# Performance work log

Hardware: AMD Instinct MI355X
Metric: run time of the kernel (lower is better)

## Reference

```python
import jax, jax.numpy as jnp
import numpy as np

NUM_CLASSES = 80
C_OUT = 81
SCORE_THR = 0.02
IOU_THR = 0.45
TOPK = 1000
IMG_MAX = 320.0
STRIDES = [16, 32, 64, 107, 160, 320]
MIN_SIZES = [48, 100, 150, 202, 253, 304]
MAX_SIZES = [100, 150, 202, 253, 304, 320]
FEAT = [20, 10, 5, 3, 2, 1]
MAX_RATIO = float(abs(np.log(0.016)))


def _base_anchors(level):
    base = float(MIN_SIZES[level])
    scales = np.array([1.0, np.sqrt(MAX_SIZES[level] / MIN_SIZES[level])])
    ratios = np.array([1.0, 0.5, 2.0, 1.0 / 3.0, 3.0])
    h_ratios = np.sqrt(ratios)
    w_ratios = 1.0 / h_ratios
    # scale_major=False: scales vary along rows
    ws = (base * scales[:, None] * w_ratios[None, :]).reshape(-1)
    hs = (base * scales[:, None] * h_ratios[None, :]).reshape(-1)
    c = STRIDES[level] / 2.0
    ba = np.stack([c - 0.5 * ws, c - 0.5 * hs, c + 0.5 * ws, c + 0.5 * hs], -1)
    return ba[[0, 5, 1, 2, 3, 4]]  # index_select reorder, 6 anchors/loc


def _priors(level):
    ba = _base_anchors(level)
    f, s = FEAT[level], STRIDES[level]
    sx = np.arange(f, dtype=np.float64) * s
    xx = np.tile(sx, f)
    yy = np.repeat(sx, f)
    shifts = np.stack([xx, yy, xx, yy], -1)  # [f*f,4]
    return (ba[None, :, :] + shifts[:, None, :]).reshape(-1, 4).astype(np.float32)


PRIORS = [jnp.asarray(_priors(i)) for i in range(6)]


def delta2bbox(priors, deltas):
    stds = jnp.array([0.1, 0.1, 0.2, 0.2], dtype=deltas.dtype)
    d = deltas * stds
    pxy = (priors[:, :2] + priors[:, 2:]) * 0.5
    pwh = priors[:, 2:] - priors[:, :2]
    dwh = jnp.clip(d[:, 2:], -MAX_RATIO, MAX_RATIO)
    gxy = pxy + pwh * d[:, :2]
    gwh = pwh * jnp.exp(dwh)
    boxes = jnp.concatenate([gxy - 0.5 * gwh, gxy + 0.5 * gwh], -1)
    return jnp.clip(boxes, 0.0, IMG_MAX)


def _nms_keep(boxes, valid, iou_thr):
    # greedy NMS over score-sorted boxes; returns bool keep mask
    K = boxes.shape[0]
    area = (boxes[:, 2] - boxes[:, 0]) * (boxes[:, 3] - boxes[:, 1])
    lt = jnp.maximum(boxes[:, None, :2], boxes[None, :, :2])
    rb = jnp.minimum(boxes[:, None, 2:], boxes[None, :, 2:])
    wh = jnp.clip(rb - lt, 0.0)
    inter = wh[..., 0] * wh[..., 1]
    iou = inter / (area[:, None] + area[None, :] - inter)
    ar = jnp.arange(K)

    def body(i, alive):
        sup = (iou[i] > iou_thr) & (ar > i) & alive[i]
        return alive & ~sup

    return jax.lax.fori_loop(0, K, body, valid)


def _single_image(cls_list, bb_list):
    boxes_l, scores_l, labels_l, valid_l = [], [], [], []
    for cls, bb, priors in zip(cls_list, bb_list, PRIORS):
        probs = jax.nn.softmax(cls.transpose(1, 2, 0).reshape(-1, C_OUT), axis=-1)[:, :NUM_CLASSES]
        flat = probs.reshape(-1)  # [N*80]
        k = min(TOPK, flat.shape[0])
        masked = jnp.where(flat > SCORE_THR, flat, -1.0)
        vals, idx = jax.lax.top_k(masked, k)
        valid = vals > SCORE_THR
        a_idx = idx // NUM_CLASSES
        lbl = idx % NUM_CLASSES
        deltas = bb.transpose(1, 2, 0).reshape(-1, 4)[a_idx]
        boxes = delta2bbox(priors[a_idx], deltas)
        boxes_l.append(boxes)
        scores_l.append(jnp.where(valid, vals, 0.0))
        labels_l.append(lbl)
        valid_l.append(valid)
    boxes = jnp.concatenate(boxes_l, 0)   # [K,4]
    scores = jnp.concatenate(scores_l, 0)
    labels = jnp.concatenate(labels_l, 0)
    valid = jnp.concatenate(valid_l, 0)

    # batched (class-aware) NMS via per-class coordinate offsets
    max_coord = boxes.max()
    offsets = labels.astype(boxes.dtype) * (max_coord + 1.0)
    boxes_nms = boxes + offsets[:, None]
    order = jnp.argsort(-jnp.where(valid, scores, -jnp.inf))
    boxes_s = boxes[order]
    scores_s = scores[order]
    labels_s = labels[order]
    valid_s = valid[order]
    keep = jax.lax.stop_gradient(
        _nms_keep(jax.lax.stop_gradient(boxes_nms[order]), valid_s, IOU_THR))
    dets = jnp.concatenate([boxes_s, scores_s[:, None]], -1) * keep[:, None].astype(boxes.dtype)
    return dets, labels_s, keep


def setup_inputs() -> dict:
    key = jax.random.key(0)
    ks = jax.random.split(key, 12)
    B = 4
    inp = {}
    for i, f in enumerate(FEAT):
        inp[f"cls{i}"] = jax.random.normal(ks[i], (B, 486, f, f), dtype=jnp.float32)
        inp[f"bb{i}"] = jax.random.normal(ks[6 + i], (B, 24, f, f), dtype=jnp.float32)
    return inp


def reference(cls0, cls1, cls2, cls3, cls4, cls5, bb0, bb1, bb2, bb3, bb4, bb5):
    def one(c0, c1, c2, c3, c4, c5, b0, b1, b2, b3, b4, b5):
        return _single_image([c0, c1, c2, c3, c4, c5], [b0, b1, b2, b3, b4, b5])
    dets, labels, keep = jax.vmap(one)(cls0, cls1, cls2, cls3, cls4, cls5,
                                       bb0, bb1, bb2, bb3, bb4, bb5)
    return dets, labels, keep
```

## Files before the change

kernel.cpp:

```cpp
#include <hip/hip_runtime.h>
#include <stdint.h>

#define NB 4
#define KTOT 5480
#define PER_IMG 258720
#define SCORE_THR 0.02f
#define IOU_THR 0.45f
#define REL_BASE 0x3CA3D70Bu
#define JCH 10
#define JSZ 548
#define ICH 11
#define NMSCAP 512

__constant__ int cFEAT[6]    = {20,10,5,3,2,1};
__constant__ int cSTRIDE[6]  = {16,32,64,107,160,320};
__constant__ int cMIN[6]     = {48,100,150,202,253,304};
__constant__ int cMAX[6]     = {100,150,202,253,304,320};
__constant__ int cNFLAT[6]   = {192000,48000,12000,4320,1920,480};
__constant__ int cFLATOFF[6] = {0,192000,240000,252000,256320,258240};
__constant__ int cKSEL[6]    = {1000,1000,1000,1000,1000,480};
__constant__ int cKOFF[6]    = {0,1000,2000,3000,4000,5000};
__constant__ double cRATIO[6] = {1.0,1.0,0.5,2.0,1.0/3.0,3.0};
__constant__ int eTLEV[14]   = {0,0,0,0,0,0,0,0,1,1,2,3,4,5};
__constant__ int eTCHK[14]   = {0,1,2,3,4,5,6,7,0,1,0,0,0,0};
__constant__ int eNCH[6]     = {8,2,1,1,1,1};

__device__ __forceinline__ unsigned long long mk_key(unsigned kb, int lev, unsigned idx) {
  return ((unsigned long long)kb << 21) |
         (unsigned long long)(0x1FFFFFu ^ (((unsigned)lev << 18) | idx));
}

__device__ __forceinline__ unsigned long long shfl64(unsigned long long x, int src) {
  int lo = __shfl((int)(unsigned)(x & 0xffffffffull), src);
  int hi = __shfl((int)(unsigned)(x >> 32), src);
  return ((unsigned long long)(unsigned)hi << 32) | (unsigned)lo;
}

__global__ __launch_bounds__(256) void k_softmax(
    const float* __restrict__ c0, const float* __restrict__ c1,
    const float* __restrict__ c2, const float* __restrict__ c3,
    const float* __restrict__ c4, const float* __restrict__ c5,
    float* __restrict__ scores, unsigned* __restrict__ ghist)
{
  int t = blockIdx.x;
  int b = t / 78, rem = t % 78;
  int lev, a, cb;
  if (rem < 42)      { lev = 0; a = rem / 7;        cb = (rem % 7) * 64; }
  else if (rem < 54) { lev = 1; a = (rem - 42) >> 1; cb = ((rem - 42) & 1) * 64; }
  else               { lev = 2 + (rem - 54) / 6; a = (rem - 54) % 6; cb = 0; }
  const float* cls = (lev==0)?c0:(lev==1)?c1:(lev==2)?c2:(lev==3)?c3:(lev==4)?c4:c5;
  int f = cFEAT[lev], ff = f * f;
  int ncell = ff - cb; if (ncell > 64) ncell = 64;

  __shared__ float tile[81 * 64];
  const float* base = cls + (size_t)(b * 486 + a * 81) * ff + cb;
  for (int t2 = threadIdx.x; t2 < 81 * 64; t2 += 256) {
    int c = t2 >> 6, cell = t2 & 63;
    if (cell < ncell)
      tile[(c << 6) | (cell ^ (c & 63))] = base[c * ff + cell];
  }
  __syncthreads();

  int lane = threadIdx.x & 63, w = threadIdx.x >> 6;
  unsigned* h = ghist + (size_t)(b * 6 + lev) * 8192;
  for (int cell = w; cell < ncell; cell += 4) {
    float v1 = tile[(lane << 6) | (cell ^ lane)];
    float v2 = (lane <= 16) ? tile[((lane + 64) << 6) | (cell ^ lane)]
                            : __uint_as_float(0xff800000u);
    float mx = fmaxf(v1, v2);
    #pragma unroll
    for (int m = 32; m; m >>= 1) mx = fmaxf(mx, __shfl_xor(mx, m));
    float e1 = expf(v1 - mx);
    float e2 = (lane <= 16) ? expf(v2 - mx) : 0.f;
    float sm = e1 + e2;
    #pragma unroll
    for (int m = 32; m; m >>= 1) sm += __shfl_xor(sm, m);
    int row = (cb + cell) * 6 + a;
    float* out = scores + (size_t)b * PER_IMG + cFLATOFF[lev] + row * 80;
    float p1 = e1 / sm;
    out[lane] = (p1 > SCORE_THR) ? p1 : -1.f;
    if (p1 > SCORE_THR)
      atomicAdd(&h[(__float_as_uint(p1) - REL_BASE) >> 13], 1u);
    if (lane < 16) {
      float p2 = e2 / sm;
      out[lane + 64] = (p2 > SCORE_THR) ? p2 : -1.f;
      if (p2 > SCORE_THR)
        atomicAdd(&h[(__float_as_uint(p2) - REL_BASE) >> 13], 1u);
    }
  }
}

__global__ __launch_bounds__(1024) void k_plan(
    const unsigned* __restrict__ ghist, unsigned* __restrict__ ctrl)
{
  int task = blockIdx.x;
  int lev = task % 6;
  int tid = threadIdx.x;
  if (lev == 5) { if (tid == 0) ctrl[task * 8] = 2u; return; }
  unsigned k = (unsigned)cKSEL[lev];
  const unsigned* h = ghist + (size_t)task * 8192;
  unsigned loc[8];
  unsigned ssum = 0;
  #pragma unroll
  for (int j = 0; j < 8; ++j) { loc[j] = h[tid * 8 + j]; ssum += loc[j]; }
  __shared__ unsigned sc[1024];
  sc[tid] = ssum;
  __syncthreads();
  for (int off = 1; off < 1024; off <<= 1) {
    unsigned cur = sc[tid];
    unsigned add = (tid + off < 1024) ? sc[tid + off] : 0u;
    __syncthreads();
    sc[tid] = cur + add;
    __syncthreads();
  }
  unsigned c = sc[0];
  if (c < k) { if (tid == 0) ctrl[task * 8] = 1u; return; }
  unsigned above = (tid == 1023) ? 0u : sc[tid + 1];
  unsigned run = above;
  #pragma unroll
  for (int j = 7; j >= 0; --j) {
    unsigned hj = loc[j];
    if (run < k && run + hj >= k) {
      ctrl[task * 8 + 0] = 0u;
      ctrl[task * 8 + 1] = (unsigned)(tid * 8 + j);
    }
    run += hj;
  }
}

__global__ __launch_bounds__(256) void k_emit2(
    const float* __restrict__ scores, unsigned* __restrict__ ctrl,
    unsigned long long* __restrict__ selkeys, unsigned long long* __restrict__ eqg)
{
  int b = blockIdx.x / 14, ent = blockIdx.x % 14;
  int lev = eTLEV[ent], chk = eTCHK[ent];
  int task = b * 6 + lev;
  int n = cNFLAT[lev];
  int tid = threadIdx.x;
  const float* s = scores + (size_t)b * PER_IMG + cFLATOFF[lev];
  unsigned long long* out = selkeys + (size_t)b * KTOT + cKOFF[lev];

  if (lev == 5) {
    for (int i = tid; i < n; i += 256) {
      float v = s[i];
      unsigned kb = (v > SCORE_THR) ? __float_as_uint(v) : 0u;
      out[i] = mk_key(kb, lev, (unsigned)i);
    }
    return;
  }

  __shared__ unsigned long long wbuf[1024];
  __shared__ unsigned long long ebuf[4096];
  __shared__ unsigned wcnt, ecnt, sbw, sbe;
  if (tid == 0) { wcnt = 0; ecnt = 0; }
  __syncthreads();

  unsigned mode = ctrl[task * 8];
  int csz = n / eNCH[lev];
  int start = chk * csz;
  const float4* s4 = (const float4*)(s + start);
  int n4 = csz >> 2;

  if (mode == 0u) {
    unsigned b1 = ctrl[task * 8 + 1];
    unsigned base_lo = REL_BASE + (b1 << 13);
    unsigned base_hi = base_lo + 8192u;
    #pragma unroll 4
    for (int i0 = tid; i0 < n4; i0 += 256) {
      float4 vv = s4[i0];
      #pragma unroll
      for (int e2 = 0; e2 < 4; ++e2) {
        float v = (e2==0)?vv.x:(e2==1)?vv.y:(e2==2)?vv.z:vv.w;
        if (v > SCORE_THR) {
          unsigned kb = __float_as_uint(v);
          unsigned idx = (unsigned)(start + i0 * 4 + e2);
          if (kb >= base_hi) {
            unsigned p = atomicAdd(&wcnt, 1u);
            if (p < 1024u) wbuf[p] = mk_key(kb, lev, idx);
          } else if (kb >= base_lo) {
            unsigned p = atomicAdd(&ecnt, 1u);
            if (p < 4096u) ebuf[p] = mk_key(kb, lev, idx);
          }
        }
      }
    }
  } else {
    #pragma unroll 4
    for (int i0 = tid; i0 < n4; i0 += 256) {
      float4 vv = s4[i0];
      #pragma unroll
      for (int e2 = 0; e2 < 4; ++e2) {
        float v = (e2==0)?vv.x:(e2==1)?vv.y:(e2==2)?vv.z:vv.w;
        if (v > SCORE_THR) {
          unsigned p = atomicAdd(&wcnt, 1u);
          if (p < 1024u) wbuf[p] = mk_key(__float_as_uint(v), lev,
                                          (unsigned)(start + i0 * 4 + e2));
        }
      }
    }
  }
  __syncthreads();
  if (tid == 0) {
    sbw = atomicAdd(&ctrl[task * 8 + 2], wcnt);
    sbe = atomicAdd(&ctrl[task * 8 + 3], ecnt);
  }
  __syncthreads();
  unsigned nw = (wcnt < 1024u) ? wcnt : 1024u;
  unsigned ne = (ecnt < 4096u) ? ecnt : 4096u;
  unsigned bw = sbw, be = sbe;
  for (unsigned t = tid; t < nw; t += 256) out[bw + t] = wbuf[t];
  for (unsigned t = tid; t < ne; t += 256) {
    unsigned g = be + t;
    if (g < 4096u) eqg[(size_t)task * 4096 + g] = ebuf[t];
  }
}

__global__ __launch_bounds__(1024) void k_finalize2(
    const float* __restrict__ scores, const unsigned* __restrict__ ctrl,
    unsigned long long* __restrict__ selkeys, const unsigned long long* __restrict__ eqg)
{
  int task = blockIdx.x;
  int b = task / 6, lev = task % 6;
  if (lev == 5) return;
  int tid = threadIdx.x;
  unsigned k = (unsigned)cKSEL[lev];
  int n = cNFLAT[lev];
  const float* s = scores + (size_t)b * PER_IMG + cFLATOFF[lev];
  unsigned long long* out = selkeys + (size_t)b * KTOT + cKOFF[lev];
  unsigned levtag = (unsigned)lev << 18;
  unsigned mode = ctrl[task * 8];

  __shared__ unsigned long long eqb[4096];
  __shared__ unsigned sc[1024];
  __shared__ unsigned sh_cnt, sh_eq, sh_byte, sh_r;

  if (mode == 0u) {
    unsigned cnt = ctrl[task * 8 + 2];
    unsigned e = ctrl[task * 8 + 3];
    unsigned need = k - cnt;
    if (e <= 4096u) {
      const unsigned long long* eq = eqg + (size_t)task * 4096;
      if (e == need) {
        for (unsigned t = tid; t < need; t += 1024) out[cnt + t] = eq[t];
        return;
      }
      unsigned P = 1; while (P < e) P <<= 1;
      for (unsigned t = tid; t < P; t += 1024) eqb[t] = (t < e) ? eq[t] : 0ull;
      __syncthreads();
      for (unsigned sz = 2; sz <= P; sz <<= 1)
        for (unsigned st = sz >> 1; st; st >>= 1) {
          for (unsigned w = tid; w < P / 2; w += 1024) {
            unsigned i = ((w & ~(st - 1)) << 1) | (w & (st - 1));
            unsigned l = i | st;
            bool up = ((i & sz) == 0);
            unsigned long long A = eqb[i], B = eqb[l];
            if ((A < B) == up) { eqb[i] = B; eqb[l] = A; }
          }
          __syncthreads();
        }
      for (unsigned t = tid; t < need; t += 1024) out[cnt + t] = eqb[t];
      return;
    }
  } else if (mode == 1u) {
    unsigned c = ctrl[task * 8 + 2];
    unsigned need = k - c;
    unsigned base = 0;
    for (int start = 0; start < n && base < need; start += 1024) {
      int i = start + tid;
      unsigned pred = (i < n && !(s[i] > SCORE_THR)) ? 1u : 0u;
      sc[tid] = pred;
      __syncthreads();
      for (int off = 1; off < 1024; off <<= 1) {
        unsigned add = (tid >= off) ? sc[tid - off] : 0u;
        unsigned v = sc[tid];
        __syncthreads();
        sc[tid] = v + add;
        __syncthreads();
      }
      unsigned incl = sc[tid];
      unsigned total = sc[1023];
      unsigned excl = incl - pred;
      if (pred && (base + excl) < need)
        out[c + base + excl] =
            (unsigned long long)(0x1FFFFFu ^ (levtag | (unsigned)i));
      __syncthreads();
      base += total;
    }
    return;
  }

  unsigned* hist = sc;
  unsigned* equ = (unsigned*)eqb;
  unsigned prefix = 0, r = k;
  for (int pass = 3; pass >= 0; --pass) {
    int shift = pass * 8;
    for (int i = tid; i < 256; i += 1024) hist[i] = 0;
    __syncthreads();
    for (int i = tid; i < n; i += 1024) {
      float v = s[i];
      unsigned kb = (v > SCORE_THR) ? __float_as_uint(v) : 0u;
      bool match = (pass == 3) || (((kb ^ prefix) >> (shift + 8)) == 0u);
      if (match) atomicAdd(&hist[(kb >> shift) & 255u], 1u);
    }
    __syncthreads();
    if (tid == 0) {
      unsigned cum = 0, byte = 0, rr = r;
      for (int bb = 255; bb >= 0; --bb) {
        unsigned hh = hist[bb];
        if (cum + hh >= r) { byte = (unsigned)bb; rr = r - cum; break; }
        cum += hh;
      }
      sh_byte = byte; sh_r = rr;
    }
    __syncthreads();
    prefix |= (sh_byte << shift);
    r = sh_r;
    __syncthreads();
  }
  unsigned Kstar = prefix;
  if (tid == 0) { sh_cnt = 0; sh_eq = 0; }
  __syncthreads();
  for (int i = tid; i < n; i += 1024) {
    float v = s[i];
    unsigned kb = (v > SCORE_THR) ? __float_as_uint(v) : 0u;
    if (kb > Kstar) {
      unsigned slot = atomicAdd(&sh_cnt, 1u);
      out[slot] = mk_key(kb, lev, (unsigned)i);
    } else if (kb == Kstar) {
      unsigned es = atomicAdd(&sh_eq, 1u);
      if (es < 4096u) equ[es] = (unsigned)i;
    }
  }
  __syncthreads();
  unsigned m = sh_cnt;
  unsigned e2 = (sh_eq < 4096u) ? sh_eq : 4096u;
  unsigned need2 = k - m;
  if (e2 > need2) {
    unsigned P = 1; while (P < e2) P <<= 1;
    for (unsigned t = tid; t < P; t += 1024) if (t >= e2) equ[t] = 0xFFFFFFFFu;
    __syncthreads();
    for (unsigned sz = 2; sz <= P; sz <<= 1)
      for (unsigned st = sz >> 1; st; st >>= 1) {
        for (unsigned w = tid; w < P / 2; w += 1024) {
          unsigned i = ((w & ~(st - 1)) << 1) | (w & (st - 1));
          unsigned l = i | st;
          bool up = ((i & sz) == 0);
          unsigned A = equ[i], B = equ[l];
          if ((A > B) == up) { equ[i] = B; equ[l] = A; }
        }
        __syncthreads();
      }
  }
  __syncthreads();
  for (unsigned t = tid; t < need2; t += 1024)
    out[m + t] = ((unsigned long long)Kstar << 21) |
                 (unsigned long long)(0x1FFFFFu ^ (levtag | equ[t]));
}

__global__ __launch_bounds__(512) void k_rank(
    const unsigned long long* __restrict__ selkeys, unsigned* __restrict__ rank_part)
{
  int blk = blockIdx.x;
  int jc = blk % JCH;
  int rest = blk / JCH;
  int ic = rest % ICH, b = rest / ICH;
  int tid = threadIdx.x;
  __shared__ __align__(16) unsigned long long sk[JSZ];
  const unsigned long long* keys = selkeys + (size_t)b * KTOT;
  for (int j = tid; j < JSZ; j += 512) sk[j] = keys[jc * JSZ + j];
  int i = ic * 512 + tid;
  unsigned long long mk = (i < KTOT) ? keys[i] : 0ull;
  __syncthreads();
  unsigned r = 0;
  const ulonglong2* sk2 = (const ulonglong2*)sk;
  #pragma unroll 8
  for (int j = 0; j < JSZ / 2; ++j) {
    ulonglong2 kk = sk2[j];
    r += (kk.x > mk) ? 1u : 0u;
    r += (kk.y > mk) ? 1u : 0u;
  }
  if (i < KTOT) rank_part[((size_t)jc * NB + b) * KTOT + i] = r;
}

__global__ __launch_bounds__(512) void k_decode(
    const unsigned long long* __restrict__ selkeys, const unsigned* __restrict__ rank_part,
    const float* __restrict__ g0, const float* __restrict__ g1,
    const float* __restrict__ g2, const float* __restrict__ g3,
    const float* __restrict__ g4, const float* __restrict__ g5,
    float* __restrict__ boxes, float* __restrict__ oscore,
    unsigned char* __restrict__ lab8, unsigned* __restrict__ obmax_u,
    float* __restrict__ outp)
{
  int b = blockIdx.x / ICH, ic = blockIdx.x % ICH;
  int tid = threadIdx.x;
  int i = ic * 512 + tid;
  __shared__ double ba[6][6][4];
  if (tid < 36) {
    int lev = tid / 6, a = tid % 6;
    double base = (double)cMIN[lev];
    double scl = (a == 1) ? sqrt((double)cMAX[lev] / (double)cMIN[lev]) : 1.0;
    double hr = sqrt(cRATIO[a]);
    double wr = 1.0 / hr;
    double wsz = base * scl * wr;
    double hsz = base * scl * hr;
    double cc = (double)cSTRIDE[lev] / 2.0;
    ba[lev][a][0] = cc - 0.5 * wsz;
    ba[lev][a][1] = cc - 0.5 * hsz;
    ba[lev][a][2] = cc + 0.5 * wsz;
    ba[lev][a][3] = cc + 0.5 * hsz;
  }
  __syncthreads();

  float lmax = 0.f;
  if (i < KTOT) {
    unsigned long long mk = selkeys[(size_t)b * KTOT + i];
    unsigned r = 0;
    #pragma unroll
    for (int jc = 0; jc < JCH; ++jc)
      r += rank_part[((size_t)jc * NB + b) * KTOT + i];
    unsigned tag = 0x1FFFFFu ^ (unsigned)(mk & 0x1FFFFFull);
    int lev = tag >> 18;
    int fi = tag & 0x3FFFF;
    unsigned vb2 = (unsigned)(mk >> 21);
    int valid = (vb2 != 0u);
    float score = valid ? __uint_as_float(vb2) : 0.f;
    int label = fi % 80;
    int arow = fi / 80;
    int a = arow % 6, cell = arow / 6;
    int f = cFEAT[lev], ff = f * f;
    int x = cell % f, y = cell / f;
    const float* gb = (lev==0)?g0:(lev==1)?g1:(lev==2)?g2:(lev==3)?g3:(lev==4)?g4:g5;
    const float* pb = gb + (size_t)(b * 24 + a * 4) * ff + y * f + x;
    float d0 = pb[0] * 0.1f, d1 = pb[ff] * 0.1f;
    float d2 = pb[2 * ff] * 0.2f, d3 = pb[3 * ff] * 0.2f;
    const float MR = (float)4.135166556742356;
    d2 = fminf(fmaxf(d2, -MR), MR);
    d3 = fminf(fmaxf(d3, -MR), MR);
    double shx = (double)(x * cSTRIDE[lev]);
    double shy = (double)(y * cSTRIDE[lev]);
    float p0 = (float)(ba[lev][a][0] + shx);
    float p1 = (float)(ba[lev][a][1] + shy);
    float p2 = (float)(ba[lev][a][2] + shx);
    float p3 = (float)(ba[lev][a][3] + shy);
    float pxc = (p0 + p2) * 0.5f, pyc = (p1 + p3) * 0.5f;
    float pw = p2 - p0, ph = p3 - p1;
    float gx = pxc + pw * d0, gy = pyc + ph * d1;
    float gw = pw * expf(d2), gh = ph * expf(d3);
    float x1 = gx - 0.5f * gw, y1 = gy - 0.5f * gh;
    float x2 = gx + 0.5f * gw, y2 = gy + 0.5f * gh;
    x1 = fminf(fmaxf(x1, 0.f), 320.f);
    y1 = fminf(fmaxf(y1, 0.f), 320.f);
    x2 = fminf(fmaxf(x2, 0.f), 320.f);
    y2 = fminf(fmaxf(y2, 0.f), 320.f);
    size_t o = (size_t)b * KTOT + (size_t)r;
    boxes[o * 4 + 0] = x1; boxes[o * 4 + 1] = y1;
    boxes[o * 4 + 2] = x2; boxes[o * 4 + 3] = y2;
    oscore[o] = score;
    lab8[o] = valid ? (unsigned char)label : (unsigned char)0xFF;
    outp[(size_t)NB * KTOT * 5 + o] = (float)label;
    if (!valid) {
      float* det = outp + o * 5;
      det[0] = 0.f; det[1] = 0.f; det[2] = 0.f; det[3] = 0.f; det[4] = 0.f;
      outp[(size_t)NB * KTOT * 6 + o] = 0.f;
    }
    lmax = fmaxf(fmaxf(x1, y1), fmaxf(x2, y2));
  }
  #pragma unroll
  for (int m = 32; m; m >>= 1) lmax = fmaxf(lmax, __shfl_xor(lmax, m));
  if ((tid & 63) == 0) atomicMax(&obmax_u[b], __float_as_uint(lmax));
}

__global__ __launch_bounds__(256) void k_nms(
    const float* __restrict__ boxes, const float* __restrict__ oscore,
    const unsigned char* __restrict__ lab8, const unsigned* __restrict__ obmax_u,
    float* __restrict__ out)
{
  int blk = blockIdx.x;
  int b = blk / 80, cls = blk % 80;
  int tid = threadIdx.x;
  int lane = tid & 63, w = tid >> 6;

  __shared__ unsigned short list[NMSCAP];
  __shared__ float ox1[NMSCAP], oy1[NMSCAP], ox2[NMSCAP], oy2[NMSCAP];
  __shared__ float oar[NMSCAP], osc[NMSCAP];
  __shared__ float rx1[NMSCAP], ry1[NMSCAP], rx2[NMSCAP], ry2[NMSCAP];
  __shared__ unsigned long long mask[NMSCAP][8];
  __shared__ unsigned ccnt[24], cbase[24];
  __shared__ int sh_n;
  __shared__ unsigned long long alive_s[8];

  float ofs = (float)cls * (__uint_as_float(obmax_u[b]) + 1.0f);
  const unsigned* lb32 = (const unsigned*)(lab8 + (size_t)b * KTOT);

  unsigned long long balA[6][4];
  #pragma unroll
  for (int ci = 0; ci < 6; ++ci) {
    int chunk = w + ci * 4;
    unsigned v = 0xFFFFFFFFu;
    if (chunk < 22) {
      int u = chunk * 64 + lane;
      if (u < KTOT / 4) v = lb32[u];
    }
    unsigned long long m0 = __ballot(((v      ) & 0xFFu) == (unsigned)cls);
    unsigned long long m1 = __ballot(((v >>  8) & 0xFFu) == (unsigned)cls);
    unsigned long long m2 = __ballot(((v >> 16) & 0xFFu) == (unsigned)cls);
    unsigned long long m3 = __ballot(((v >> 24) & 0xFFu) == (unsigned)cls);
    balA[ci][0] = m0; balA[ci][1] = m1; balA[ci][2] = m2; balA[ci][3] = m3;
    if (chunk < 22 && lane == 0)
      ccnt[chunk] = (unsigned)(__popcll(m0) + __popcll(m1) + __popcll(m2) + __popcll(m3));
  }
  __syncthreads();
  if (tid == 0) {
    unsigned tot = 0;
    for (int c = 0; c < 22; ++c) { cbase[c] = tot; tot += ccnt[c]; }
    sh_n = (tot < NMSCAP) ? (int)tot : NMSCAP;
  }
  __syncthreads();
  int n = sh_n;
  unsigned long long blt = (lane == 0) ? 0ull : ((~0ull) >> (64 - lane));
  #pragma unroll
  for (int ci = 0; ci < 6; ++ci) {
    int chunk = w + ci * 4;
    if (chunk < 22) {
      unsigned pos = cbase[chunk];
      unsigned below = (unsigned)(__popcll(balA[ci][0] & blt) + __popcll(balA[ci][1] & blt) +
                                  __popcll(balA[ci][2] & blt) + __popcll(balA[ci][3] & blt));
      unsigned within = 0;
      #pragma unroll
      for (int k = 0; k < 4; ++k) {
        if ((balA[ci][k] >> lane) & 1ull) {
          unsigned mypos = pos + below + within;
          if (mypos < NMSCAP) list[mypos] = (unsigned short)(chunk * 256 + lane * 4 + k);
          ++within;
        }
      }
    }
  }
  __syncthreads();

  for (int t = tid; t < n; t += 256) {
    int pos = list[t];
    size_t o = (size_t)b * KTOT + pos;
    float4 bb = *(const float4*)(boxes + o * 4);
    rx1[t] = bb.x; ry1[t] = bb.y; rx2[t] = bb.z; ry2[t] = bb.w;
    float a1 = bb.x + ofs, b1 = bb.y + ofs, a2 = bb.z + ofs, b2 = bb.w + ofs;
    ox1[t] = a1; oy1[t] = b1; ox2[t] = a2; oy2[t] = b2;
    oar[t] = (a2 - a1) * (b2 - b1);
    osc[t] = oscore[o];
  }
  __syncthreads();

  int nw = (n + 63) >> 6;
  for (int i = tid; i < n; i += 256) {
    float ax1 = ox1[i], ay1 = oy1[i], ax2 = ox2[i], ay2 = oy2[i], aar = oar[i];
    int w0 = i >> 6;
    for (int wd = w0; wd < nw; ++wd) {
      unsigned long long m = 0;
      int jbase = wd << 6;
      int jend = n - jbase; if (jend > 64) jend = 64;
      for (int jj = 0; jj < jend; ++jj) {
        int j = jbase + jj;
        if (j > i) {
          float ix1 = fmaxf(ax1, ox1[j]);
          float iy1 = fmaxf(ay1, oy1[j]);
          float ix2 = fminf(ax2, ox2[j]);
          float iy2 = fminf(ay2, oy2[j]);
          float iw = fmaxf(ix2 - ix1, 0.f);
          float ih = fmaxf(iy2 - iy1, 0.f);
          float inter = iw * ih;
          float iou = inter / (aar + oar[j] - inter);
          if (iou > IOU_THR) m |= (1ull << jj);
        }
      }
      mask[i][wd] = m;
    }
  }
  __syncthreads();

  if (w == 0) {
    unsigned long long aw = 0;
    if (lane < nw) {
      int rem = n - (lane << 6);
      aw = (rem >= 64) ? ~0ull : ((1ull << rem) - 1ull);
    }
    for (int i = 0; i < n; ++i) {
      int wi = i >> 6;
      unsigned long long mrow = (lane >= wi && lane < nw) ? mask[i][lane] : 0ull;
      unsigned long long tw = shfl64(aw, wi);
      if ((tw >> (i & 63)) & 1ull) aw &= ~mrow;
    }
    if (lane < 8) alive_s[lane] = aw;
  }
  __syncthreads();

  for (int t = tid; t < n; t += 256) {
    float kf = ((alive_s[t >> 6] >> (t & 63)) & 1ull) ? 1.f : 0.f;
    int pos = list[t];
    size_t o = (size_t)b * KTOT + pos;
    float* det = out + o * 5;
    det[0] = rx1[t] * kf; det[1] = ry1[t] * kf;
    det[2] = rx2[t] * kf; det[3] = ry2[t] * kf;
    det[4] = osc[t] * kf;
    out[(size_t)NB * KTOT * 6 + o] = kf;
  }
}

extern "C" void kernel_launch(void* const* d_in, const int* in_sizes, int n_in,
                              void* d_out, int out_size, void* d_ws, size_t ws_size,
                              hipStream_t stream) {
  (void)in_sizes; (void)n_in; (void)out_size; (void)ws_size;
  const float* cls[6]; const float* bbx[6];
  for (int i = 0; i < 6; ++i) {
    cls[i] = (const float*)d_in[2 * i];
    bbx[i] = (const float*)d_in[2 * i + 1];
  }
  char* ws = (char*)d_ws;
  float* scores = (float*)ws;
  unsigned* rank_part = (unsigned*)ws;
  unsigned long long* selkeys = (unsigned long long*)(ws + 4139520);
  float* boxes  = (float*)(ws + 4314880);
  float* oscore = (float*)(ws + 4665600);
  unsigned char* lab8 = (unsigned char*)(ws + 4753280);
  unsigned* obmax_u = (unsigned*)(ws + 5016320);
  unsigned* ghist = (unsigned*)(ws + 5016576);
  unsigned* ctrl  = (unsigned*)(ws + 5803008);
  unsigned long long* eqg = (unsigned long long*)(ws + 5803776);

  hipMemsetAsync(ws + 5016320, 0, 787456, stream);
  k_softmax<<<NB * 78, 256, 0, stream>>>(cls[0], cls[1], cls[2], cls[3], cls[4], cls[5],
                                         scores, ghist);
  k_plan<<<24, 1024, 0, stream>>>(ghist, ctrl);
  k_emit2<<<NB * 14, 256, 0, stream>>>(scores, ctrl, selkeys, eqg);
  k_finalize2<<<24, 1024, 0, stream>>>(scores, ctrl, selkeys, eqg);
  k_rank<<<NB * ICH * JCH, 512, 0, stream>>>(selkeys, rank_part);
  k_decode<<<NB * ICH, 512, 0, stream>>>(selkeys, rank_part, bbx[0], bbx[1], bbx[2],
                                         bbx[3], bbx[4], bbx[5], boxes, oscore, lab8,
                                         obmax_u, (float*)d_out);
  k_nms<<<NB * 80, 256, 0, stream>>>(boxes, oscore, lab8, obmax_u, (float*)d_out);
}
```

Before: 113.2 us.

## Fuse pipeline into one cooperative persistent kernel with grid syncs

Replaces the memset and seven separate kernel launches with a single cooperative kernel of 256 blocks that runs each stage in a loop and separates stages with grid-wide syncs. Workspace zeroing moves into the kernel, and the plan stage is folded into emit by recomputing the histogram threshold per block. Block sizes drop from 512/1024 to 256 threads. This aims to remove launch gaps and memset overhead, at the cost of grid-barrier latency, less parallelism in some stages, and a large shared-memory union that may limit occupancy.

```diff
diff --git a/kernel.cpp b/kernel.cpp
--- a/kernel.cpp
+++ b/kernel.cpp
@@ -1,5 +1,8 @@
 #include <hip/hip_runtime.h>
+#include <hip/hip_cooperative_groups.h>
 #include <stdint.h>
+
+namespace cg = cooperative_groups;
 
 #define NB 4
 #define KTOT 5480
@@ -9,8 +12,9 @@
 #define REL_BASE 0x3CA3D70Bu
 #define JCH 10
 #define JSZ 548
-#define ICH 11
 #define NMSCAP 512
+#define ZN4 49216
+#define NBLK 256
 
 __constant__ int cFEAT[6]    = {20,10,5,3,2,1};
 __constant__ int cSTRIDE[6]  = {16,32,64,107,160,320};
@@ -36,572 +40,584 @@
   return ((unsigned long long)(unsigned)hi << 32) | (unsigned)lo;
 }
 
-__global__ __launch_bounds__(256) void k_softmax(
-    const float* __restrict__ c0, const float* __restrict__ c1,
-    const float* __restrict__ c2, const float* __restrict__ c3,
-    const float* __restrict__ c4, const float* __restrict__ c5,
-    float* __restrict__ scores, unsigned* __restrict__ ghist)
+struct SmemSM { float tile[81 * 64]; };
+struct SmemEM {
+  unsigned long long wbuf[1024];
+  unsigned long long ebuf[4096];
+  unsigned sc[256];
+  unsigned wcnt, ecnt, sbw, sbe, smode, sb1;
+};
+struct SmemFN {
+  unsigned long long eqb[4096];
+  unsigned sc[256];
+  unsigned cntS, eqS, byteS, rS;
+};
+struct SmemRK { unsigned long long sk[JSZ]; };
+struct SmemDC { double ba[6][6][4]; };
+struct SmemNM {
+  unsigned long long mask[NMSCAP][8];
+  float ox1[NMSCAP], oy1[NMSCAP], ox2[NMSCAP], oy2[NMSCAP];
+  float oar[NMSCAP], osc[NMSCAP];
+  float rx1[NMSCAP], ry1[NMSCAP], rx2[NMSCAP], ry2[NMSCAP];
+  unsigned short list[NMSCAP];
+  unsigned ccnt[24], cbase[24];
+  unsigned long long alive[8];
+  int n;
+};
+union SmemU {
+  SmemSM sm; SmemEM em; SmemFN fn; SmemRK rk; SmemDC dc; SmemNM nm;
+};
+
+__global__ void __launch_bounds__(256) k_mega(
+    const float* c0, const float* c1, const float* c2,
+    const float* c3, const float* c4, const float* c5,
+    const float* g0, const float* g1, const float* g2,
+    const float* g3, const float* g4, const float* g5,
+    float* scores, unsigned long long* selkeys, float* boxes, float* oscore,
+    unsigned char* lab8, unsigned* obmax_u, unsigned* ghist, unsigned* ctrl,
+    unsigned long long* eqg, unsigned* rank_part, float* outp, float4* zbase)
 {
-  int t = blockIdx.x;
-  int b = t / 78, rem = t % 78;
-  int lev, a, cb;
-  if (rem < 42)      { lev = 0; a = rem / 7;        cb = (rem % 7) * 64; }
-  else if (rem < 54) { lev = 1; a = (rem - 42) >> 1; cb = ((rem - 42) & 1) * 64; }
-  else               { lev = 2 + (rem - 54) / 6; a = (rem - 54) % 6; cb = 0; }
-  const float* cls = (lev==0)?c0:(lev==1)?c1:(lev==2)?c2:(lev==3)?c3:(lev==4)?c4:c5;
-  int f = cFEAT[lev], ff = f * f;
-  int ncell = ff - cb; if (ncell > 64) ncell = 64;
-
-  __shared__ float tile[81 * 64];
-  const float* base = cls + (size_t)(b * 486 + a * 81) * ff + cb;
-  for (int t2 = threadIdx.x; t2 < 81 * 64; t2 += 256) {
-    int c = t2 >> 6, cell = t2 & 63;
-    if (cell < ncell)
-      tile[(c << 6) | (cell ^ (c & 63))] = base[c * ff + cell];
+  cg::grid_group gg = cg::this_grid();
+  __shared__ SmemU smem;
+  const int tid = threadIdx.x;
+  const int blk = blockIdx.x;
+
+  {
+    int i = blk * 256 + tid;
+    if (i < ZN4) zbase[i] = make_float4(0.f, 0.f, 0.f, 0.f);
   }
-  __syncthreads();
-
-  int lane = threadIdx.x & 63, w = threadIdx.x >> 6;
-  unsigned* h = ghist + (size_t)(b * 6 + lev) * 8192;
-  for (int cell = w; cell < ncell; cell += 4) {
-    float v1 = tile[(lane << 6) | (cell ^ lane)];
-    float v2 = (lane <= 16) ? tile[((lane + 64) << 6) | (cell ^ lane)]
-                            : __uint_as_float(0xff800000u);
-    float mx = fmaxf(v1, v2);
+  gg.sync();
+
+  for (int t = blk; t < NB * 78; t += NBLK) {
+    __syncthreads();
+    int b = t / 78, rem = t % 78;
+    int lev, a, cb;
+    if (rem < 42)      { lev = 0; a = rem / 7;         cb = (rem % 7) * 64; }
+    else if (rem < 54) { lev = 1; a = (rem - 42) >> 1; cb = ((rem - 42) & 1) * 64; }
+    else               { lev = 2 + (rem - 54) / 6; a = (rem - 54) % 6; cb = 0; }
+    const float* cls = (lev==0)?c0:(lev==1)?c1:(lev==2)?c2:(lev==3)?c3:(lev==4)?c4:c5;
+    int f = cFEAT[lev], ff = f * f;
+    int ncell = ff - cb; if (ncell > 64) ncell = 64;
+    const float* base = cls + (size_t)(b * 486 + a * 81) * ff + cb;
+    for (int t2 = tid; t2 < 81 * 64; t2 += 256) {
+      int c = t2 >> 6, cell = t2 & 63;
+      if (cell < ncell)
+        smem.sm.tile[(c << 6) | (cell ^ (c & 63))] = base[c * ff + cell];
+    }
+    __syncthreads();
+    int lane = tid & 63, w = tid >> 6;
+    unsigned* h = ghist + (size_t)(b * 6 + lev) * 8192;
+    for (int cell = w; cell < ncell; cell += 4) {
+      float v1 = smem.sm.tile[(lane << 6) | (cell ^ lane)];
+      float v2 = (lane <= 16) ? smem.sm.tile[((lane + 64) << 6) | (cell ^ lane)]
+                              : __uint_as_float(0xff800000u);
+      float mx = fmaxf(v1, v2);
+      #pragma unroll
+      for (int m = 32; m; m >>= 1) mx = fmaxf(mx, __shfl_xor(mx, m));
+      float e1 = expf(v1 - mx);
+      float e2 = (lane <= 16) ? expf(v2 - mx) : 0.f;
+      float sm = e1 + e2;
+      #pragma unroll
+      for (int m = 32; m; m >>= 1) sm += __shfl_xor(sm, m);
+      int row = (cb + cell) * 6 + a;
+      float* outs = scores + (size_t)b * PER_IMG + cFLATOFF[lev] + row * 80;
+      float p1 = e1 / sm;
+      outs[lane] = (p1 > SCORE_THR) ? p1 : -1.f;
+      if (p1 > SCORE_THR)
+        atomicAdd(&h[(__float_as_uint(p1) - REL_BASE) >> 13], 1u);
+      if (lane < 16) {
+        float p2 = e2 / sm;
+        outs[lane + 64] = (p2 > SCORE_THR) ? p2 : -1.f;
+        if (p2 > SCORE_THR)
+          atomicAdd(&h[(__float_as_uint(p2) - REL_BASE) >> 13], 1u);
+      }
+    }
+  }
+  gg.sync();
+
+  if (blk < NB * 14) {
+    int b = blk / 14, ent = blk % 14;
+    int lev = eTLEV[ent], chk = eTCHK[ent];
+    int task = b * 6 + lev;
+    int n = cNFLAT[lev];
+    const float* s = scores + (size_t)b * PER_IMG + cFLATOFF[lev];
+    unsigned long long* outk = selkeys + (size_t)b * KTOT + cKOFF[lev];
+    if (lev == 5) {
+      for (int i = tid; i < n; i += 256) {
+        float v = s[i];
+        unsigned kb = (v > SCORE_THR) ? __float_as_uint(v) : 0u;
+        outk[i] = mk_key(kb, lev, (unsigned)i);
+      }
+    } else {
+      unsigned kk = (unsigned)cKSEL[lev];
+      {
+        const unsigned* h = ghist + (size_t)task * 8192;
+        unsigned loc[32]; unsigned ssum = 0;
+        #pragma unroll
+        for (int j = 0; j < 32; ++j) { loc[j] = h[tid * 32 + j]; ssum += loc[j]; }
+        smem.em.sc[tid] = ssum;
+        __syncthreads();
+        for (int off = 1; off < 256; off <<= 1) {
+          unsigned cur = smem.em.sc[tid];
+          unsigned add = (tid + off < 256) ? smem.em.sc[tid + off] : 0u;
+          __syncthreads();
+          smem.em.sc[tid] = cur + add;
+          __syncthreads();
+        }
+        unsigned call = smem.em.sc[0];
+        if (call < kk) { if (tid == 0) smem.em.smode = 1u; }
+        else {
+          unsigned above = (tid == 255) ? 0u : smem.em.sc[tid + 1];
+          unsigned run = above;
+          #pragma unroll
+          for (int j = 31; j >= 0; --j) {
+            unsigned hj = loc[j];
+            if (run < kk && run + hj >= kk) {
+              smem.em.smode = 0u; smem.em.sb1 = (unsigned)(tid * 32 + j);
+            }
+            run += hj;
+          }
+        }
+        __syncthreads();
+      }
+      unsigned mode = smem.em.smode;
+      unsigned b1 = (mode == 0u) ? smem.em.sb1 : 0u;
+      if (tid == 0) { smem.em.wcnt = 0; smem.em.ecnt = 0; }
+      __syncthreads();
+      int csz = n / eNCH[lev];
+      int start = chk * csz;
+      const float4* s4 = (const float4*)(s + start);
+      int n4 = csz >> 2;
+      if (mode == 0u) {
+        unsigned base_lo = REL_BASE + (b1 << 13);
+        unsigned base_hi = base_lo + 8192u;
+        #pragma unroll 4
+        for (int i0 = tid; i0 < n4; i0 += 256) {
+          float4 vv = s4[i0];
+          #pragma unroll
+          for (int e2 = 0; e2 < 4; ++e2) {
+            float v = (e2==0)?vv.x:(e2==1)?vv.y:(e2==2)?vv.z:vv.w;
+            if (v > SCORE_THR) {
+              unsigned kb = __float_as_uint(v);
+              unsigned idx = (unsigned)(start + i0 * 4 + e2);
+              if (kb >= base_hi) {
+                unsigned p = atomicAdd(&smem.em.wcnt, 1u);
+                if (p < 1024u) smem.em.wbuf[p] = mk_key(kb, lev, idx);
+              } else if (kb >= base_lo) {
+                unsigned p = atomicAdd(&smem.em.ecnt, 1u);
+                if (p < 4096u) smem.em.ebuf[p] = mk_key(kb, lev, idx);
+              }
+            }
+          }
+        }
+      } else {
+        #pragma unroll 4
+        for (int i0 = tid; i0 < n4; i0 += 256) {
+          float4 vv = s4[i0];
+          #pragma unroll
+          for (int e2 = 0; e2 < 4; ++e2) {
+            float v = (e2==0)?vv.x:(e2==1)?vv.y:(e2==2)?vv.z:vv.w;
+            if (v > SCORE_THR) {
+              unsigned p = atomicAdd(&smem.em.wcnt, 1u);
+              if (p < 1024u) smem.em.wbuf[p] = mk_key(__float_as_uint(v), lev,
+                                                      (unsigned)(start + i0 * 4 + e2));
+            }
+          }
+        }
+      }
+      __syncthreads();
+      if (tid == 0) {
+        smem.em.sbw = atomicAdd(&ctrl[task * 8 + 2], smem.em.wcnt);
+        smem.em.sbe = atomicAdd(&ctrl[task * 8 + 3], smem.em.ecnt);
+      }
+      __syncthreads();
+      unsigned nw = (smem.em.wcnt < 1024u) ? smem.em.wcnt : 1024u;
+      unsigned ne = (smem.em.ecnt < 4096u) ? smem.em.ecnt : 4096u;
+      unsigned bw = smem.em.sbw, be = smem.em.sbe;
+      for (unsigned t = tid; t < nw; t += 256) outk[bw + t] = smem.em.wbuf[t];
+      for (unsigned t = tid; t < ne; t += 256) {
+        unsigned g = be + t;
+        if (g < 4096u) eqg[(size_t)task * 4096 + g] = smem.em.ebuf[t];
+      }
+    }
+  }
+  gg.sync();
+
+  if (blk < NB * 6) {
+    int task = blk;
+    int b = task / 6, lev = task % 6;
+    if (lev != 5) {
+      unsigned kk = (unsigned)cKSEL[lev];
+      int n = cNFLAT[lev];
+      const float* s = scores + (size_t)b * PER_IMG + cFLATOFF[lev];
+      unsigned long long* outk = selkeys + (size_t)b * KTOT + cKOFF[lev];
+      unsigned levtag = (unsigned)lev << 18;
+      const unsigned* h = ghist + (size_t)task * 8192;
+      unsigned ssum = 0;
+      #pragma unroll
+      for (int j = 0; j < 32; ++j) ssum += h[tid * 32 + j];
+      smem.fn.sc[tid] = ssum;
+      __syncthreads();
+      for (int off = 128; off >= 1; off >>= 1) {
+        if (tid < off) smem.fn.sc[tid] += smem.fn.sc[tid + off];
+        __syncthreads();
+      }
+      unsigned call = smem.fn.sc[0];
+      __syncthreads();
+      unsigned mode = (call >= kk) ? 0u : 1u;
+      bool done = false;
+
+      if (mode == 0u) {
+        unsigned cnt = ctrl[task * 8 + 2];
+        unsigned e = ctrl[task * 8 + 3];
+        unsigned need = kk - cnt;
+        if (e <= 4096u) {
+          const unsigned long long* eq = eqg + (size_t)task * 4096;
+          if (e == need) {
+            for (unsigned t = tid; t < need; t += 256) outk[cnt + t] = eq[t];
+          } else {
+            unsigned P = 1; while (P < e) P <<= 1;
+            for (unsigned t = tid; t < P; t += 256)
+              smem.fn.eqb[t] = (t < e) ? eq[t] : 0ull;
+            __syncthreads();
+            for (unsigned sz = 2; sz <= P; sz <<= 1)
+              for (unsigned st = sz >> 1; st; st >>= 1) {
+                for (unsigned w2 = tid; w2 < P / 2; w2 += 256) {
+                  unsigned i = ((w2 & ~(st - 1)) << 1) | (w2 & (st - 1));
+                  unsigned l = i | st;
+                  bool up = ((i & sz) == 0);
+                  unsigned long long A = smem.fn.eqb[i], B = smem.fn.eqb[l];
+                  if ((A < B) == up) { smem.fn.eqb[i] = B; smem.fn.eqb[l] = A; }
+                }
+                __syncthreads();
+              }
+            for (unsigned t = tid; t < need; t += 256) outk[cnt + t] = smem.fn.eqb[t];
+          }
+          done = true;
+        }
+      } else {
+        unsigned c = ctrl[task * 8 + 2];
+        unsigned need = kk - c;
+        unsigned base = 0;
+        for (int start = 0; start < n && base < need; start += 256) {
+          int i = start + tid;
+          unsigned pred = (i < n && !(s[i] > SCORE_THR)) ? 1u : 0u;
+          smem.fn.sc[tid] = pred;
+          __syncthreads();
+          for (int off = 1; off < 256; off <<= 1) {
+            unsigned add = (tid >= off) ? smem.fn.sc[tid - off] : 0u;
+            unsigned v = smem.fn.sc[tid];
+            __syncthreads();
+            smem.fn.sc[tid] = v + add;
+            __syncthreads();
+          }
+          unsigned incl = smem.fn.sc[tid];
+          unsigned total = smem.fn.sc[255];
+          unsigned excl = incl - pred;
+          if (pred && (base + excl) < need)
+            outk[c + base + excl] =
+                (unsigned long long)(0x1FFFFFu ^ (levtag | (unsigned)i));
+          __syncthreads();
+          base += total;
+        }
+        done = true;
+      }
+
+      if (!done) {
+        unsigned* hist = smem.fn.sc;
+        unsigned* equ = (unsigned*)smem.fn.eqb;
+        unsigned prefix = 0, r = kk;
+        for (int pass = 3; pass >= 0; --pass) {
+          int shift = pass * 8;
+          hist[tid] = 0;
+          __syncthreads();
+          for (int i = tid; i < n; i += 256) {
+            float v = s[i];
+            unsigned kb = (v > SCORE_THR) ? __float_as_uint(v) : 0u;
+            bool match = (pass == 3) || (((kb ^ prefix) >> (shift + 8)) == 0u);
+            if (match) atomicAdd(&hist[(kb >> shift) & 255u], 1u);
+          }
+          __syncthreads();
+          if (tid == 0) {
+            unsigned cum = 0, byte = 0, rr = r;
+            for (int bb = 255; bb >= 0; --bb) {
+              unsigned hh = hist[bb];
+              if (cum + hh >= r) { byte = (unsigned)bb; rr = r - cum; break; }
+              cum += hh;
+            }
+            smem.fn.byteS = byte; smem.fn.rS = rr;
+          }
+          __syncthreads();
+          prefix |= (smem.fn.byteS << shift);
+          r = smem.fn.rS;
+          __syncthreads();
+        }
+        unsigned Kstar = prefix;
+        if (tid == 0) { smem.fn.cntS = 0; smem.fn.eqS = 0; }
+        __syncthreads();
+        for (int i = tid; i < n; i += 256) {
+          float v = s[i];
+          unsigned kb = (v > SCORE_THR) ? __float_as_uint(v) : 0u;
+          if (kb > Kstar) {
+            unsigned slot = atomicAdd(&smem.fn.cntS, 1u);
+            outk[slot] = mk_key(kb, lev, (unsigned)i);
+          } else if (kb == Kstar) {
+            unsigned es = atomicAdd(&smem.fn.eqS, 1u);
+            if (es < 4096u) equ[es] = (unsigned)i;
+          }
+        }
+        __syncthreads();
+        unsigned m = smem.fn.cntS;
+        unsigned e2 = (smem.fn.eqS < 4096u) ? smem.fn.eqS : 4096u;
+        unsigned need2 = kk - m;
+        if (e2 > need2) {
+          unsigned P = 1; while (P < e2) P <<= 1;
+          for (unsigned t = tid; t < P; t += 256) if (t >= e2) equ[t] = 0xFFFFFFFFu;
+          __syncthreads();
+          for (unsigned sz = 2; sz <= P; sz <<= 1)
+            for (unsigned st = sz >> 1; st; st >>= 1) {
+              for (unsigned w2 = tid; w2 < P / 2; w2 += 256) {
+                unsigned i = ((w2 & ~(st - 1)) << 1) | (w2 & (st - 1));
+                unsigned l = i | st;
+                bool up = ((i & sz) == 0);
+                unsigned A = equ[i], B = equ[l];
+                if ((A > B) == up) { equ[i] = B; equ[l] = A; }
+              }
+              __syncthreads();
+            }
+        }
+        __syncthreads();
+        for (unsigned t = tid; t < need2; t += 256)
+          outk[m + t] = ((unsigned long long)Kstar << 21) |
+                        (unsigned long long)(0x1FFFFFu ^ (levtag | equ[t]));
+      }
+    }
+  }
+  gg.sync();
+
+  for (int t = blk; t < NB * 22 * JCH; t += NBLK) {
+    int jc = t % JCH;
+    int rest = t / JCH;
+    int ic = rest % 22, b = rest / 22;
+    __syncthreads();
+    const unsigned long long* keys = selkeys + (size_t)b * KTOT;
+    for (int j = tid; j < JSZ; j += 256) smem.rk.sk[j] = keys[jc * JSZ + j];
+    int i = ic * 256 + tid;
+    unsigned long long mk = (i < KTOT) ? keys[i] : 0ull;
+    __syncthreads();
+    unsigned r = 0;
+    const ulonglong2* sk2 = (const ulonglong2*)smem.rk.sk;
+    #pragma unroll 8
+    for (int j = 0; j < JSZ / 2; ++j) {
+      ulonglong2 kk2 = sk2[j];
+      r += (kk2.x > mk) ? 1u : 0u;
+      r += (kk2.y > mk) ? 1u : 0u;
+    }
+    if (i < KTOT) rank_part[((size_t)jc * NB + b) * KTOT + i] = r;
+  }
+  gg.sync();
+
+  if (blk < NB * 22) {
+    int b = blk / 22, ic = blk % 22;
+    int i = ic * 256 + tid;
+    if (tid < 36) {
+      int lev = tid / 6, a = tid % 6;
+      double base = (double)cMIN[lev];
+      double scl = (a == 1) ? sqrt((double)cMAX[lev] / (double)cMIN[lev]) : 1.0;
+      double hr = sqrt(cRATIO[a]);
+      double wr = 1.0 / hr;
+      double wsz = base * scl * wr;
+      double hsz = base * scl * hr;
+      double cc = (double)cSTRIDE[lev] / 2.0;
+      smem.dc.ba[lev][a][0] = cc - 0.5 * wsz;
+      smem.dc.ba[lev][a][1] = cc - 0.5 * hsz;
+      smem.dc.ba[lev][a][2] = cc + 0.5 * wsz;
+      smem.dc.ba[lev][a][3] = cc + 0.5 * hsz;
+    }
+    __syncthreads();
+    float lmax = 0.f;
+    if (i < KTOT) {
+      unsigned long long mk = selkeys[(size_t)b * KTOT + i];
+      unsigned r = 0;
+      #pragma unroll
+      for (int jc = 0; jc < JCH; ++jc)
+        r += rank_part[((size_t)jc * NB + b) * KTOT + i];
+      unsigned tag = 0x1FFFFFu ^ (unsigned)(mk & 0x1FFFFFull);
+      int lev = tag >> 18;
+      int fi = tag & 0x3FFFF;
+      unsigned vb2 = (unsigned)(mk >> 21);
+      int valid = (vb2 != 0u);
+      float score = valid ? __uint_as_float(vb2) : 0.f;
+      int label = fi % 80;
+      int arow = fi / 80;
+      int a = arow % 6, cell = arow / 6;
+      int f = cFEAT[lev], ff = f * f;
+      int x = cell % f, y = cell / f;
+      const float* gb = (lev==0)?g0:(lev==1)?g1:(lev==2)?g2:(lev==3)?g3:(lev==4)?g4:g5;
+      const float* pb = gb + (size_t)(b * 24 + a * 4) * ff + y * f + x;
+      float d0 = pb[0] * 0.1f, d1 = pb[ff] * 0.1f;
+      float d2 = pb[2 * ff] * 0.2f, d3 = pb[3 * ff] * 0.2f;
+      const float MR = (float)4.135166556742356;
+      d2 = fminf(fmaxf(d2, -MR), MR);
+      d3 = fminf(fmaxf(d3, -MR), MR);
+      double shx = (double)(x * cSTRIDE[lev]);
+      double shy = (double)(y * cSTRIDE[lev]);
+      float p0 = (float)(smem.dc.ba[lev][a][0] + shx);
+      float p1 = (float)(smem.dc.ba[lev][a][1] + shy);
+      float p2 = (float)(smem.dc.ba[lev][a][2] + shx);
+      float p3 = (float)(smem.dc.ba[lev][a][3] + shy);
+      float pxc = (p0 + p2) * 0.5f, pyc = (p1 + p3) * 0.5f;
+      float pw = p2 - p0, ph = p3 - p1;
+      float gx = pxc + pw * d0, gy = pyc + ph * d1;
+      float gw = pw * expf(d2), gh = ph * expf(d3);
+      float x1 = gx - 0.5f * gw, y1 = gy - 0.5f * gh;
+      float x2 = gx + 0.5f * gw, y2 = gy + 0.5f * gh;
+      x1 = fminf(fmaxf(x1, 0.f), 320.f);
+      y1 = fminf(fmaxf(y1, 0.f), 320.f);
+      x2 = fminf(fmaxf(x2, 0.f), 320.f);
+      y2 = fminf(fmaxf(y2, 0.f), 320.f);
+      size_t o = (size_t)b * KTOT + (size_t)r;
+      boxes[o * 4 + 0] = x1; boxes[o * 4 + 1] = y1;
+      boxes[o * 4 + 2] = x2; boxes[o * 4 + 3] = y2;
+      oscore[o] = score;
+      lab8[o] = valid ? (unsigned char)label : (unsigned char)0xFF;
+      outp[(size_t)NB * KTOT * 5 + o] = (float)label;
+      if (!valid) {
+        float* det = outp + o * 5;
+        det[0] = 0.f; det[1] = 0.f; det[2] = 0.f; det[3] = 0.f; det[4] = 0.f;
+        outp[(size_t)NB * KTOT * 6 + o] = 0.f;
+      }
+      lmax = fmaxf(fmaxf(x1, y1), fmaxf(x2, y2));
+    }
     #pragma unroll
-    for (int m = 32; m; m >>= 1) mx = fmaxf(mx, __shfl_xor(mx, m));
-    float e1 = expf(v1 - mx);
-    float e2 = (lane <= 16) ? expf(v2 - mx) : 0.f;
-    float sm = e1 + e2;
+    for (int m = 32; m; m >>= 1) lmax = fmaxf(lmax, __shfl_xor(lmax, m));
+    if ((tid & 63) == 0) atomicMax(&obmax_u[b], __float_as_uint(lmax));
+  }
+  gg.sync();
+
+  for (int t0 = blk; t0 < NB * 80; t0 += NBLK) {
+    __syncthreads();
+    int b = t0 / 80, cls2 = t0 % 80;
+    int lane = tid & 63, w = tid >> 6;
+    float ofs = (float)cls2 * (__uint_as_float(obmax_u[b]) + 1.0f);
+    const unsigned* lb32 = (const unsigned*)(lab8 + (size_t)b * KTOT);
+
+    unsigned long long balA[6][4];
     #pragma unroll
-    for (int m = 32; m; m >>= 1) sm += __shfl_xor(sm, m);
-    int row = (cb + cell) * 6 + a;
-    float* out = scores + (size_t)b * PER_IMG + cFLATOFF[lev] + row * 80;
-    float p1 = e1 / sm;
-    out[lane] = (p1 > SCORE_THR) ? p1 : -1.f;
-    if (p1 > SCORE_THR)
-      atomicAdd(&h[(__float_as_uint(p1) - REL_BASE) >> 13], 1u);
-    if (lane < 16) {
-      float p2 = e2 / sm;
-      out[lane + 64] = (p2 > SCORE_THR) ? p2 : -1.f;
-      if (p2 > SCORE_THR)
-        atomicAdd(&h[(__float_as_uint(p2) - REL_BASE) >> 13], 1u);
-    }
-  }
-}
-
-__global__ __launch_bounds__(1024) void k_plan(
-    const unsigned* __restrict__ ghist, unsigned* __restrict__ ctrl)
-{
-  int task = blockIdx.x;
-  int lev = task % 6;
-  int tid = threadIdx.x;
-  if (lev == 5) { if (tid == 0) ctrl[task * 8] = 2u; return; }
-  unsigned k = (unsigned)cKSEL[lev];
-  const unsigned* h = ghist + (size_t)task * 8192;
-  unsigned loc[8];
-  unsigned ssum = 0;
-  #pragma unroll
-  for (int j = 0; j < 8; ++j) { loc[j] = h[tid * 8 + j]; ssum += loc[j]; }
-  __shared__ unsigned sc[1024];
-  sc[tid] = ssum;
-  __syncthreads();
-  for (int off = 1; off < 1024; off <<= 1) {
-    unsigned cur = sc[tid];
-    unsigned add = (tid + off < 1024) ? sc[tid + off] : 0u;
-    __syncthreads();
-    sc[tid] = cur + add;
-    __syncthreads();
-  }
-  unsigned c = sc[0];
-  if (c < k) { if (tid == 0) ctrl[task * 8] = 1u; return; }
-  unsigned above = (tid == 1023) ? 0u : sc[tid + 1];
-  unsigned run = above;
-  #pragma unroll
-  for (int j = 7; j >= 0; --j) {
-    unsigned hj = loc[j];
-    if (run < k && run + hj >= k) {
-      ctrl[task * 8 + 0] = 0u;
-      ctrl[task * 8 + 1] = (unsigned)(tid * 8 + j);
-    }
-    run += hj;
-  }
-}
-
-__global__ __launch_bounds__(256) void k_emit2(
-    const float* __restrict__ scores, unsigned* __restrict__ ctrl,
-    unsigned long long* __restrict__ selkeys, unsigned long long* __restrict__ eqg)
-{
-  int b = blockIdx.x / 14, ent = blockIdx.x % 14;
-  int lev = eTLEV[ent], chk = eTCHK[ent];
-  int task = b * 6 + lev;
-  int n = cNFLAT[lev];
-  int tid = threadIdx.x;
-  const float* s = scores + (size_t)b * PER_IMG + cFLATOFF[lev];
-  unsigned long long* out = selkeys + (size_t)b * KTOT + cKOFF[lev];
-
-  if (lev == 5) {
-    for (int i = tid; i < n; i += 256) {
-      float v = s[i];
-      unsigned kb = (v > SCORE_THR) ? __float_as_uint(v) : 0u;
-      out[i] = mk_key(kb, lev, (unsigned)i);
-    }
-    return;
-  }
-
-  __shared__ unsigned long long wbuf[1024];
-  __shared__ unsigned long long ebuf[4096];
-  __shared__ unsigned wcnt, ecnt, sbw, sbe;
-  if (tid == 0) { wcnt = 0; ecnt = 0; }
-  __syncthreads();
-
-  unsigned mode = ctrl[task * 8];
-  int csz = n / eNCH[lev];
-  int start = chk * csz;
-  const float4* s4 = (const float4*)(s + start);
-  int n4 = csz >> 2;
-
-  if (mode == 0u) {
-    unsigned b1 = ctrl[task * 8 + 1];
-    unsigned base_lo = REL_BASE + (b1 << 13);
-    unsigned base_hi = base_lo + 8192u;
-    #pragma unroll 4
-    for (int i0 = tid; i0 < n4; i0 += 256) {
-      float4 vv = s4[i0];
-      #pragma unroll
-      for (int e2 = 0; e2 < 4; ++e2) {
-        float v = (e2==0)?vv.x:(e2==1)?vv.y:(e2==2)?vv.z:vv.w;
-        if (v > SCORE_THR) {
-          unsigned kb = __float_as_uint(v);
-          unsigned idx = (unsigned)(start + i0 * 4 + e2);
-          if (kb >= base_hi) {
-            unsigned p = atomicAdd(&wcnt, 1u);
-            if (p < 1024u) wbuf[p] = mk_key(kb, lev, idx);
-          } else if (kb >= base_lo) {
-            unsigned p = atomicAdd(&ecnt, 1u);
-            if (p < 4096u) ebuf[p] = mk_key(kb, lev, idx);
-          }
-        }
-      }
-    }
-  } else {
-    #pragma unroll 4
-    for (int i0 = tid; i0 < n4; i0 += 256) {
-      float4 vv = s4[i0];
-      #pragma unroll
-      for (int e2 = 0; e2 < 4; ++e2) {
-        float v = (e2==0)?vv.x:(e2==1)?vv.y:(e2==2)?vv.z:vv.w;
-        if (v > SCORE_THR) {
-          unsigned p = atomicAdd(&wcnt, 1u);
-          if (p < 1024u) wbuf[p] = mk_key(__float_as_uint(v), lev,
-                                          (unsigned)(start + i0 * 4 + e2));
-        }
-      }
-    }
-  }
-  __syncthreads();
-  if (tid == 0) {
-    sbw = atomicAdd(&ctrl[task * 8 + 2], wcnt);
-    sbe = atomicAdd(&ctrl[task * 8 + 3], ecnt);
-  }
-  __syncthreads();
-  unsigned nw = (wcnt < 1024u) ? wcnt : 1024u;
-  unsigned ne = (ecnt < 4096u) ? ecnt : 4096u;
-  unsigned bw = sbw, be = sbe;
-  for (unsigned t = tid; t < nw; t += 256) out[bw + t] = wbuf[t];
-  for (unsigned t = tid; t < ne; t += 256) {
-    unsigned g = be + t;
-    if (g < 4096u) eqg[(size_t)task * 4096 + g] = ebuf[t];
-  }
-}
-
-__global__ __launch_bounds__(1024) void k_finalize2(
-    const float* __restrict__ scores, const unsigned* __restrict__ ctrl,
-    unsigned long long* __restrict__ selkeys, const unsigned long long* __restrict__ eqg)
-{
-  int task = blockIdx.x;
-  int b = task / 6, lev = task % 6;
-  if (lev == 5) return;
-  int tid = threadIdx.x;
-  unsigned k = (unsigned)cKSEL[lev];
-  int n = cNFLAT[lev];
-  const float* s = scores + (size_t)b * PER_IMG + cFLATOFF[lev];
-  unsigned long long* out = selkeys + (size_t)b * KTOT + cKOFF[lev];
-  unsigned levtag = (unsigned)lev << 18;
-  unsigned mode = ctrl[task * 8];
-
-  __shared__ unsigned long long eqb[4096];
-  __shared__ unsigned sc[1024];
-  __shared__ unsigned sh_cnt, sh_eq, sh_byte, sh_r;
-
-  if (mode == 0u) {
-    unsigned cnt = ctrl[task * 8 + 2];
-    unsigned e = ctrl[task * 8 + 3];
-    unsigned need = k - cnt;
-    if (e <= 4096u) {
-      const unsigned long long* eq = eqg + (size_t)task * 4096;
-      if (e == need) {
-        for (unsigned t = tid; t < need; t += 1024) out[cnt + t] = eq[t];
-        return;
-      }
-      unsigned P = 1; while (P < e) P <<= 1;
-      for (unsigned t = tid; t < P; t += 1024) eqb[t] = (t < e) ? eq[t] : 0ull;
-      __syncthreads();
-      for (unsigned sz = 2; sz <= P; sz <<= 1)
-        for (unsigned st = sz >> 1; st; st >>= 1) {
-          for (unsigned w = tid; w < P / 2; w += 1024) {
-            unsigned i = ((w & ~(st - 1)) << 1) | (w & (st - 1));
-            unsigned l = i | st;
-            bool up = ((i & sz) == 0);
-            unsigned long long A = eqb[i], B = eqb[l];
-            if ((A < B) == up) { eqb[i] = B; eqb[l] = A; }
-          }
-          __syncthreads();
-        }
-      for (unsigned t = tid; t < need; t += 1024) out[cnt + t] = eqb[t];
-      return;
-    }
-  } else if (mode == 1u) {
-    unsigned c = ctrl[task * 8 + 2];
-    unsigned need = k - c;
-    unsigned base = 0;
-    for (int start = 0; start < n && base < need; start += 1024) {
-      int i = start + tid;
-      unsigned pred = (i < n && !(s[i] > SCORE_THR)) ? 1u : 0u;
-      sc[tid] = pred;
-      __syncthreads();
-      for (int off = 1; off < 1024; off <<= 1) {
-        unsigned add = (tid >= off) ? sc[tid - off] : 0u;
-        unsigned v = sc[tid];
-        __syncthreads();
-        sc[tid] = v + add;
-        __syncthreads();
-      }
-      unsigned incl = sc[tid];
-      unsigned total = sc[1023];
-      unsigned excl = incl - pred;
-      if (pred && (base + excl) < need)
-        out[c + base + excl] =
-            (unsigned long long)(0x1FFFFFu ^ (levtag | (unsigned)i));
-      __syncthreads();
-      base += total;
-    }
-    return;
-  }
-
-  unsigned* hist = sc;
-  unsigned* equ = (unsigned*)eqb;
-  unsigned prefix = 0, r = k;
-  for (int pass = 3; pass >= 0; --pass) {
-    int shift = pass * 8;
-    for (int i = tid; i < 256; i += 1024) hist[i] = 0;
-    __syncthreads();
-    for (int i = tid; i < n; i += 1024) {
-      float v = s[i];
-      unsigned kb = (v > SCORE_THR) ? __float_as_uint(v) : 0u;
-      bool match = (pass == 3) || (((kb ^ prefix) >> (shift + 8)) == 0u);
-      if (match) atomicAdd(&hist[(kb >> shift) & 255u], 1u);
+    for (int ci = 0; ci < 6; ++ci) {
+      int chunk = w + ci * 4;
+      unsigned v = 0xFFFFFFFFu;
+      if (chunk < 22) {
+        int u = chunk * 64 + lane;
+        if (u < KTOT / 4) v = lb32[u];
+      }
+      unsigned long long m0 = __ballot(((v      ) & 0xFFu) == (unsigned)cls2);
+      unsigned long long m1 = __ballot(((v >>  8) & 0xFFu) == (unsigned)cls2);
+      unsigned long long m2 = __ballot(((v >> 16) & 0xFFu) == (unsigned)cls2);
+      unsigned long long m3 = __ballot(((v >> 24) & 0xFFu) == (unsigned)cls2);
+      balA[ci][0] = m0; balA[ci][1] = m1; balA[ci][2] = m2; balA[ci][3] = m3;
+      if (chunk < 22 && lane == 0)
+        smem.nm.ccnt[chunk] =
+            (unsigned)(__popcll(m0) + __popcll(m1) + __popcll(m2) + __popcll(m3));
     }
     __syncthreads();
     if (tid == 0) {
-      unsigned cum = 0, byte = 0, rr = r;
-      for (int bb = 255; bb >= 0; --bb) {
-        unsigned hh = hist[bb];
-        if (cum + hh >= r) { byte = (unsigned)bb; rr = r - cum; break; }
-        cum += hh;
-      }
-      sh_byte = byte; sh_r = rr;
-    }
-    __syncthreads();
-    prefix |= (sh_byte << shift);
-    r = sh_r;
-    __syncthreads();
-  }
-  unsigned Kstar = prefix;
-  if (tid == 0) { sh_cnt = 0; sh_eq = 0; }
-  __syncthreads();
-  for (int i = tid; i < n; i += 1024) {
-    float v = s[i];
-    unsigned kb = (v > SCORE_THR) ? __float_as_uint(v) : 0u;
-    if (kb > Kstar) {
-      unsigned slot = atomicAdd(&sh_cnt, 1u);
-      out[slot] = mk_key(kb, lev, (unsigned)i);
-    } else if (kb == Kstar) {
-      unsigned es = atomicAdd(&sh_eq, 1u);
-      if (es < 4096u) equ[es] = (unsigned)i;
-    }
-  }
-  __syncthreads();
-  unsigned m = sh_cnt;
-  unsigned e2 = (sh_eq < 4096u) ? sh_eq : 4096u;
-  unsigned need2 = k - m;
-  if (e2 > need2) {
-    unsigned P = 1; while (P < e2) P <<= 1;
-    for (unsigned t = tid; t < P; t += 1024) if (t >= e2) equ[t] = 0xFFFFFFFFu;
-    __syncthreads();
-    for (unsigned sz = 2; sz <= P; sz <<= 1)
-      for (unsigned st = sz >> 1; st; st >>= 1) {
-        for (unsigned w = tid; w < P / 2; w += 1024) {
-          unsigned i = ((w & ~(st - 1)) << 1) | (w & (st - 1));
-          unsigned l = i | st;
-          bool up = ((i & sz) == 0);
-          unsigned A = equ[i], B = equ[l];
-          if ((A > B) == up) { equ[i] = B; equ[l] = A; }
-        }
-        __syncthreads();
-      }
-  }
-  __syncthreads();
-  for (unsigned t = tid; t < need2; t += 1024)
-    out[m + t] = ((unsigned long long)Kstar << 21) |
-                 (unsigned long long)(0x1FFFFFu ^ (levtag | equ[t]));
-}
-
-__global__ __launch_bounds__(512) void k_rank(
-    const unsigned long long* __restrict__ selkeys, unsigned* __restrict__ rank_part)
-{
-  int blk = blockIdx.x;
-  int jc = blk % JCH;
-  int rest = blk / JCH;
-  int ic = rest % ICH, b = rest / ICH;
-  int tid = threadIdx.x;
-  __shared__ __align__(16) unsigned long long sk[JSZ];
-  const unsigned long long* keys = selkeys + (size_t)b * KTOT;
-  for (int j = tid; j < JSZ; j += 512) sk[j] = keys[jc * JSZ + j];
-  int i = ic * 512 + tid;
-  unsigned long long mk = (i < KTOT) ? keys[i] : 0ull;
-  __syncthreads();
-  unsigned r = 0;
-  const ulonglong2* sk2 = (const ulonglong2*)sk;
-  #pragma unroll 8
-  for (int j = 0; j < JSZ / 2; ++j) {
-    ulonglong2 kk = sk2[j];
-    r += (kk.x > mk) ? 1u : 0u;
-    r += (kk.y > mk) ? 1u : 0u;
-  }
-  if (i < KTOT) rank_part[((size_t)jc * NB + b) * KTOT + i] = r;
-}
-
-__global__ __launch_bounds__(512) void k_decode(
-    const unsigned long long* __restrict__ selkeys, const unsigned* __restrict__ rank_part,
-    const float* __restrict__ g0, const float* __restrict__ g1,
-    const float* __restrict__ g2, const float* __restrict__ g3,
-    const float* __restrict__ g4, const float* __restrict__ g5,
-    float* __restrict__ boxes, float* __restrict__ oscore,
-    unsigned char* __restrict__ lab8, unsigned* __restrict__ obmax_u,
-    float* __restrict__ outp)
-{
-  int b = blockIdx.x / ICH, ic = blockIdx.x % ICH;
-  int tid = threadIdx.x;
-  int i = ic * 512 + tid;
-  __shared__ double ba[6][6][4];
-  if (tid < 36) {
-    int lev = tid / 6, a = tid % 6;
-    double base = (double)cMIN[lev];
-    double scl = (a == 1) ? sqrt((double)cMAX[lev] / (double)cMIN[lev]) : 1.0;
-    double hr = sqrt(cRATIO[a]);
-    double wr = 1.0 / hr;
-    double wsz = base * scl * wr;
-    double hsz = base * scl * hr;
-    double cc = (double)cSTRIDE[lev] / 2.0;
-    ba[lev][a][0] = cc - 0.5 * wsz;
-    ba[lev][a][1] = cc - 0.5 * hsz;
-    ba[lev][a][2] = cc + 0.5 * wsz;
-    ba[lev][a][3] = cc + 0.5 * hsz;
-  }
-  __syncthreads();
-
-  float lmax = 0.f;
-  if (i < KTOT) {
-    unsigned long long mk = selkeys[(size_t)b * KTOT + i];
-    unsigned r = 0;
+      unsigned tot = 0;
+      for (int c = 0; c < 22; ++c) { smem.nm.cbase[c] = tot; tot += smem.nm.ccnt[c]; }
+      smem.nm.n = (tot < NMSCAP) ? (int)tot : NMSCAP;
+    }
+    __syncthreads();
+    int nn = smem.nm.n;
+    unsigned long long blt = (lane == 0) ? 0ull : ((~0ull) >> (64 - lane));
     #pragma unroll
-    for (int jc = 0; jc < JCH; ++jc)
-      r += rank_part[((size_t)jc * NB + b) * KTOT + i];
-    unsigned tag = 0x1FFFFFu ^ (unsigned)(mk & 0x1FFFFFull);
-    int lev = tag >> 18;
-    int fi = tag & 0x3FFFF;
-    unsigned vb2 = (unsigned)(mk >> 21);
-    int valid = (vb2 != 0u);
-    float score = valid ? __uint_as_float(vb2) : 0.f;
-    int label = fi % 80;
-    int arow = fi / 80;
-    int a = arow % 6, cell = arow / 6;
-    int f = cFEAT[lev], ff = f * f;
-    int x = cell % f, y = cell / f;
-    const float* gb = (lev==0)?g0:(lev==1)?g1:(lev==2)?g2:(lev==3)?g3:(lev==4)?g4:g5;
-    const float* pb = gb + (size_t)(b * 24 + a * 4) * ff + y * f + x;
-    float d0 = pb[0] * 0.1f, d1 = pb[ff] * 0.1f;
-    float d2 = pb[2 * ff] * 0.2f, d3 = pb[3 * ff] * 0.2f;
-    const float MR = (float)4.135166556742356;
-    d2 = fminf(fmaxf(d2, -MR), MR);
-    d3 = fminf(fmaxf(d3, -MR), MR);
-    double shx = (double)(x * cSTRIDE[lev]);
-    double shy = (double)(y * cSTRIDE[lev]);
-    float p0 = (float)(ba[lev][a][0] + shx);
-    float p1 = (float)(ba[lev][a][1] + shy);
-    float p2 = (float)(ba[lev][a][2] + shx);
-    float p3 = (float)(ba[lev][a][3] + shy);
-    float pxc = (p0 + p2) * 0.5f, pyc = (p1 + p3) * 0.5f;
-    float pw = p2 - p0, ph = p3 - p1;
-    float gx = pxc + pw * d0, gy = pyc + ph * d1;
-    float gw = pw * expf(d2), gh = ph * expf(d3);
-    float x1 = gx - 0.5f * gw, y1 = gy - 0.5f * gh;
-    float x2 = gx + 0.5f * gw, y2 = gy + 0.5f * gh;
-    x1 = fminf(fmaxf(x1, 0.f), 320.f);
-    y1 = fminf(fmaxf(y1, 0.f), 320.f);
-    x2 = fminf(fmaxf(x2, 0.f), 320.f);
-    y2 = fminf(fmaxf(y2, 0.f), 320.f);
-    size_t o = (size_t)b * KTOT + (size_t)r;
-    boxes[o * 4 + 0] = x1; boxes[o * 4 + 1] = y1;
-    boxes[o * 4 + 2] = x2; boxes[o * 4 + 3] = y2;
-    oscore[o] = score;
-    lab8[o] = valid ? (unsigned char)label : (unsigned char)0xFF;
-    outp[(size_t)NB * KTOT * 5 + o] = (float)label;
-    if (!valid) {
+    for (int ci = 0; ci < 6; ++ci) {
+      int chunk = w + ci * 4;
+      if (chunk < 22) {
+        unsigned pos = smem.nm.cbase[chunk];
+        unsigned below = (unsigned)(__popcll(balA[ci][0] & blt) + __popcll(balA[ci][1] & blt) +
+                                    __popcll(balA[ci][2] & blt) + __popcll(balA[ci][3] & blt));
+        unsigned within = 0;
+        #pragma unroll
+        for (int k2 = 0; k2 < 4; ++k2) {
+          if ((balA[ci][k2] >> lane) & 1ull) {
+            unsigned mypos = pos + below + within;
+            if (mypos < NMSCAP)
+              smem.nm.list[mypos] = (unsigned short)(chunk * 256 + lane * 4 + k2);
+            ++within;
+          }
+        }
+      }
+    }
+    __syncthreads();
+
+    for (int t = tid; t < nn; t += 256) {
+      int pos = smem.nm.list[t];
+      size_t o = (size_t)b * KTOT + pos;
+      float4 bb = *(const float4*)(boxes + o * 4);
+      smem.nm.rx1[t] = bb.x; smem.nm.ry1[t] = bb.y;
+      smem.nm.rx2[t] = bb.z; smem.nm.ry2[t] = bb.w;
+      float a1 = bb.x + ofs, b1 = bb.y + ofs, a2 = bb.z + ofs, b2 = bb.w + ofs;
+      smem.nm.ox1[t] = a1; smem.nm.oy1[t] = b1;
+      smem.nm.ox2[t] = a2; smem.nm.oy2[t] = b2;
+      smem.nm.oar[t] = (a2 - a1) * (b2 - b1);
+      smem.nm.osc[t] = oscore[o];
+    }
+    __syncthreads();
+
+    int nw = (nn + 63) >> 6;
+    for (int i = tid; i < nn; i += 256) {
+      float ax1 = smem.nm.ox1[i], ay1 = smem.nm.oy1[i];
+      float ax2 = smem.nm.ox2[i], ay2 = smem.nm.oy2[i], aar = smem.nm.oar[i];
+      int w0 = i >> 6;
+      for (int wd = w0; wd < nw; ++wd) {
+        unsigned long long m = 0;
+        int jbase = wd << 6;
+        int jend = nn - jbase; if (jend > 64) jend = 64;
+        for (int jj = 0; jj < jend; ++jj) {
+          int j = jbase + jj;
+          if (j > i) {
+            float ix1 = fmaxf(ax1, smem.nm.ox1[j]);
+            float iy1 = fmaxf(ay1, smem.nm.oy1[j]);
+            float ix2 = fminf(ax2, smem.nm.ox2[j]);
+            float iy2 = fminf(ay2, smem.nm.oy2[j]);
+            float iw = fmaxf(ix2 - ix1, 0.f);
+            float ih = fmaxf(iy2 - iy1, 0.f);
+            float inter = iw * ih;
+            float iou = inter / (aar + smem.nm.oar[j] - inter);
+            if (iou > IOU_THR) m |= (1ull << jj);
+          }
+        }
+        smem.nm.mask[i][wd] = m;
+      }
+    }
+    __syncthreads();
+
+    if (w == 0) {
+      unsigned long long aw = 0;
+      if (lane < nw) {
+        int rem = nn - (lane << 6);
+        aw = (rem >= 64) ? ~0ull : ((1ull << rem) - 1ull);
+      }
+      for (int i = 0; i < nn; ++i) {
+        int wi = i >> 6;
+        unsigned long long mrow = (lane >= wi && lane < nw) ? smem.nm.mask[i][lane] : 0ull;
+        unsigned long long tw = shfl64(aw, wi);
+        if ((tw >> (i & 63)) & 1ull) aw &= ~mrow;
+      }
+      if (lane < 8) smem.nm.alive[lane] = aw;
+    }
+    __syncthreads();
+
+    for (int t = tid; t < nn; t += 256) {
+      float kf = ((smem.nm.alive[t >> 6] >> (t & 63)) & 1ull) ? 1.f : 0.f;
+      int pos = smem.nm.list[t];
+      size_t o = (size_t)b * KTOT + pos;
       float* det = outp + o * 5;
-      det[0] = 0.f; det[1] = 0.f; det[2] = 0.f; det[3] = 0.f; det[4] = 0.f;
-      outp[(size_t)NB * KTOT * 6 + o] = 0.f;
-    }
-    lmax = fmaxf(fmaxf(x1, y1), fmaxf(x2, y2));
-  }
-  #pragma unroll
-  for (int m = 32; m; m >>= 1) lmax = fmaxf(lmax, __shfl_xor(lmax, m));
-  if ((tid & 63) == 0) atomicMax(&obmax_u[b], __float_as_uint(lmax));
-}
-
-__global__ __launch_bounds__(256) void k_nms(
-    const float* __restrict__ boxes, const float* __restrict__ oscore,
-    const unsigned char* __restrict__ lab8, const unsigned* __restrict__ obmax_u,
-    float* __restrict__ out)
-{
-  int blk = blockIdx.x;
-  int b = blk / 80, cls = blk % 80;
-  int tid = threadIdx.x;
-  int lane = tid & 63, w = tid >> 6;
-
-  __shared__ unsigned short list[NMSCAP];
-  __shared__ float ox1[NMSCAP], oy1[NMSCAP], ox2[NMSCAP], oy2[NMSCAP];
-  __shared__ float oar[NMSCAP], osc[NMSCAP];
-  __shared__ float rx1[NMSCAP], ry1[NMSCAP], rx2[NMSCAP], ry2[NMSCAP];
-  __shared__ unsigned long long mask[NMSCAP][8];
-  __shared__ unsigned ccnt[24], cbase[24];
-  __shared__ int sh_n;
-  __shared__ unsigned long long alive_s[8];
-
-  float ofs = (float)cls * (__uint_as_float(obmax_u[b]) + 1.0f);
-  const unsigned* lb32 = (const unsigned*)(lab8 + (size_t)b * KTOT);
-
-  unsigned long long balA[6][4];
-  #pragma unroll
-  for (int ci = 0; ci < 6; ++ci) {
-    int chunk = w + ci * 4;
-    unsigned v = 0xFFFFFFFFu;
-    if (chunk < 22) {
-      int u = chunk * 64 + lane;
-      if (u < KTOT / 4) v = lb32[u];
-    }
-    unsigned long long m0 = __ballot(((v      ) & 0xFFu) == (unsigned)cls);
-    unsigned long long m1 = __ballot(((v >>  8) & 0xFFu) == (unsigned)cls);
-    unsigned long long m2 = __ballot(((v >> 16) & 0xFFu) == (unsigned)cls);
-    unsigned long long m3 = __ballot(((v >> 24) & 0xFFu) == (unsigned)cls);
-    balA[ci][0] = m0; balA[ci][1] = m1; balA[ci][2] = m2; balA[ci][3] = m3;
-    if (chunk < 22 && lane == 0)
-      ccnt[chunk] = (unsigned)(__popcll(m0) + __popcll(m1) + __popcll(m2) + __popcll(m3));
-  }
-  __syncthreads();
-  if (tid == 0) {
-    unsigned tot = 0;
-    for (int c = 0; c < 22; ++c) { cbase[c] = tot; tot += ccnt[c]; }
-    sh_n = (tot < NMSCAP) ? (int)tot : NMSCAP;
-  }
-  __syncthreads();
-  int n = sh_n;
-  unsigned long long blt = (lane == 0) ? 0ull : ((~0ull) >> (64 - lane));
-  #pragma unroll
-  for (int ci = 0; ci < 6; ++ci) {
-    int chunk = w + ci * 4;
-    if (chunk < 22) {
-      unsigned pos = cbase[chunk];
-      unsigned below = (unsigned)(__popcll(balA[ci][0] & blt) + __popcll(balA[ci][1] & blt) +
-                                  __popcll(balA[ci][2] & blt) + __popcll(balA[ci][3] & blt));
-      unsigned within = 0;
-      #pragma unroll
-      for (int k = 0; k < 4; ++k) {
-        if ((balA[ci][k] >> lane) & 1ull) {
-          unsigned mypos = pos + below + within;
-          if (mypos < NMSCAP) list[mypos] = (unsigned short)(chunk * 256 + lane * 4 + k);
-          ++within;
-        }
-      }
-    }
-  }
-  __syncthreads();
-
-  for (int t = tid; t < n; t += 256) {
-    int pos = list[t];
-    size_t o = (size_t)b * KTOT + pos;
-    float4 bb = *(const float4*)(boxes + o * 4);
-    rx1[t] = bb.x; ry1[t] = bb.y; rx2[t] = bb.z; ry2[t] = bb.w;
-    float a1 = bb.x + ofs, b1 = bb.y + ofs, a2 = bb.z + ofs, b2 = bb.w + ofs;
-    ox1[t] = a1; oy1[t] = b1; ox2[t] = a2; oy2[t] = b2;
-    oar[t] = (a2 - a1) * (b2 - b1);
-    osc[t] = oscore[o];
-  }
-  __syncthreads();
-
-  int nw = (n + 63) >> 6;
-  for (int i = tid; i < n; i += 256) {
-    float ax1 = ox1[i], ay1 = oy1[i], ax2 = ox2[i], ay2 = oy2[i], aar = oar[i];
-    int w0 = i >> 6;
-    for (int wd = w0; wd < nw; ++wd) {
-      unsigned long long m = 0;
-      int jbase = wd << 6;
-      int jend = n - jbase; if (jend > 64) jend = 64;
-      for (int jj = 0; jj < jend; ++jj) {
-        int j = jbase + jj;
-        if (j > i) {
-          float ix1 = fmaxf(ax1, ox1[j]);
-          float iy1 = fmaxf(ay1, oy1[j]);
-          float ix2 = fminf(ax2, ox2[j]);
-          float iy2 = fminf(ay2, oy2[j]);
-          float iw = fmaxf(ix2 - ix1, 0.f);
-          float ih = fmaxf(iy2 - iy1, 0.f);
-          float inter = iw * ih;
-          float iou = inter / (aar + oar[j] - inter);
-          if (iou > IOU_THR) m |= (1ull << jj);
-        }
-      }
-      mask[i][wd] = m;
-    }
-  }
-  __syncthreads();
-
-  if (w == 0) {
-    unsigned long long aw = 0;
-    if (lane < nw) {
-      int rem = n - (lane << 6);
-      aw = (rem >= 64) ? ~0ull : ((1ull << rem) - 1ull);
-    }
-    for (int i = 0; i < n; ++i) {
-      int wi = i >> 6;
-      unsigned long long mrow = (lane >= wi && lane < nw) ? mask[i][lane] : 0ull;
-      unsigned long long tw = shfl64(aw, wi);
-      if ((tw >> (i & 63)) & 1ull) aw &= ~mrow;
-    }
-    if (lane < 8) alive_s[lane] = aw;
-  }
-  __syncthreads();
-
-  for (int t = tid; t < n; t += 256) {
-    float kf = ((alive_s[t >> 6] >> (t & 63)) & 1ull) ? 1.f : 0.f;
-    int pos = list[t];
-    size_t o = (size_t)b * KTOT + pos;
-    float* det = out + o * 5;
-    det[0] = rx1[t] * kf; det[1] = ry1[t] * kf;
-    det[2] = rx2[t] * kf; det[3] = ry2[t] * kf;
-    det[4] = osc[t] * kf;
-    out[(size_t)NB * KTOT * 6 + o] = kf;
+      det[0] = smem.nm.rx1[t] * kf; det[1] = smem.nm.ry1[t] * kf;
+      det[2] = smem.nm.rx2[t] * kf; det[3] = smem.nm.ry2[t] * kf;
+      det[4] = smem.nm.osc[t] * kf;
+      outp[(size_t)NB * KTOT * 6 + o] = kf;
+    }
   }
 }
 
@@ -609,11 +625,19 @@
                               void* d_out, int out_size, void* d_ws, size_t ws_size,
                               hipStream_t stream) {
   (void)in_sizes; (void)n_in; (void)out_size; (void)ws_size;
-  const float* cls[6]; const float* bbx[6];
-  for (int i = 0; i < 6; ++i) {
-    cls[i] = (const float*)d_in[2 * i];
-    bbx[i] = (const float*)d_in[2 * i + 1];
-  }
+  const float* c0 = (const float*)d_in[0];
+  const float* g0 = (const float*)d_in[1];
+  const float* c1 = (const float*)d_in[2];
+  const float* g1 = (const float*)d_in[3];
+  const float* c2 = (const float*)d_in[4];
+  const float* g2 = (const float*)d_in[5];
+  const float* c3 = (const float*)d_in[6];
+  const float* g3 = (const float*)d_in[7];
+  const float* c4 = (const float*)d_in[8];
+  const float* g4 = (const float*)d_in[9];
+  const float* c5 = (const float*)d_in[10];
+  const float* g5 = (const float*)d_in[11];
+
   char* ws = (char*)d_ws;
   float* scores = (float*)ws;
   unsigned* rank_part = (unsigned*)ws;
@@ -625,16 +649,16 @@
   unsigned* ghist = (unsigned*)(ws + 5016576);
   unsigned* ctrl  = (unsigned*)(ws + 5803008);
   unsigned long long* eqg = (unsigned long long*)(ws + 5803776);
-
-  hipMemsetAsync(ws + 5016320, 0, 787456, stream);
-  k_softmax<<<NB * 78, 256, 0, stream>>>(cls[0], cls[1], cls[2], cls[3], cls[4], cls[5],
-                                         scores, ghist);
-  k_plan<<<24, 1024, 0, stream>>>(ghist, ctrl);
-  k_emit2<<<NB * 14, 256, 0, stream>>>(scores, ctrl, selkeys, eqg);
-  k_finalize2<<<24, 1024, 0, stream>>>(scores, ctrl, selkeys, eqg);
-  k_rank<<<NB * ICH * JCH, 512, 0, stream>>>(selkeys, rank_part);
-  k_decode<<<NB * ICH, 512, 0, stream>>>(selkeys, rank_part, bbx[0], bbx[1], bbx[2],
-                                         bbx[3], bbx[4], bbx[5], boxes, oscore, lab8,
-                                         obmax_u, (float*)d_out);
-  k_nms<<<NB * 80, 256, 0, stream>>>(boxes, oscore, lab8, obmax_u, (float*)d_out);
+  float* outp = (float*)d_out;
+  float4* zbase = (float4*)(ws + 5016320);
+
+  void* args[] = {
+    (void*)&c0, (void*)&c1, (void*)&c2, (void*)&c3, (void*)&c4, (void*)&c5,
+    (void*)&g0, (void*)&g1, (void*)&g2, (void*)&g3, (void*)&g4, (void*)&g5,
+    (void*)&scores, (void*)&selkeys, (void*)&boxes, (void*)&oscore,
+    (void*)&lab8, (void*)&obmax_u, (void*)&ghist, (void*)&ctrl,
+    (void*)&eqg, (void*)&rank_part, (void*)&outp, (void*)&zbase
+  };
+  hipLaunchCooperativeKernel((const void*)k_mega, dim3(NBLK), dim3(256),
+                             args, 0, stream);
 }
```

Result: slower. 307.7 us (+171.9%).
